# Performance work log

Hardware: AMD Instinct MI355X
Metric: run time of the kernel (lower is better)

## Reference

```python
import jax, jax.numpy as jnp
import numpy as np
import math

B, N, F, H = 16, 256, 1024, 16
HD = F // H  # head_dim = 64
NEG = -9e15


def setup_inputs() -> dict:
    key = jax.random.key(0)
    ks = jax.random.split(key, 12)
    s = 0.02
    return {
        "obj_feats": jax.random.normal(ks[0], (B, N, F), jnp.float32),
        "cross_feats": jax.random.normal(ks[1], (B, N, F), jnp.float32),
        "adj_matrix": jax.random.randint(ks[2], (B, N, N), 0, 2, jnp.int32),
        "label_biases_att": jax.random.normal(ks[3], (B, N, N), jnp.float32),
        "Wq": jax.random.normal(ks[4], (F, F), jnp.float32) * s,
        "bq": jnp.zeros((F,), jnp.float32),
        "Wk": jax.random.normal(ks[5], (F, F), jnp.float32) * s,
        "bk": jnp.zeros((F,), jnp.float32),
        "Wv": jax.random.normal(ks[6], (F, F), jnp.float32) * s,
        "bv": jnp.zeros((F,), jnp.float32),
        # grouped 1x1 conv: out=F, groups=H, in_per_group=F -> weight [F, F]
        "Wo": jax.random.normal(ks[7], (F, F), jnp.float32) * s,
        "bo": jnp.zeros((F,), jnp.float32),
    }


def reference(obj_feats, cross_feats, adj_matrix, label_biases_att,
              Wq, bq, Wk, bk, Wv, bv, Wo, bo):
    # projections (torch Linear: x @ W.T + b)
    q = (jnp.einsum('bnf,gf->bng', obj_feats, Wq) + bq).reshape(B, N, H, HD)
    k = (jnp.einsum('bnf,gf->bng', cross_feats, Wk) + bk).reshape(B, N, H, HD)
    v = jnp.einsum('bnf,gf->bng', cross_feats, Wv) + bv          # [B, N, F] (NOT split per head)

    scale = 1.0 / math.sqrt(float(HD))
    att = jnp.einsum('bqhd,bkhd->bqhk', q, k) * scale            # [B, Nq, H, Nk]

    # adjacency mask broadcast over heads + label bias (both indexed [b, q, k])
    mask = (adj_matrix > 0)[:, :, None, :]                       # [B, Nq, 1, Nk]
    att = jnp.where(mask, att, NEG) + label_biases_att[:, :, None, :]

    p = jax.nn.softmax(att, axis=-1)                             # softmax over keys

    # weighted sum against un-split values: [B, Nq, H, Nk] x [B, Nk, F]
    out = jnp.einsum('bqhk,bkf->bqhf', p, v)                     # [B, Nq, H, F]

    # grouped 1x1 conv: group h maps its F input channels -> HD output channels
    Wo_g = Wo.reshape(H, HD, F)
    out = jnp.einsum('bqhf,hdf->bqhd', out, Wo_g) + bo.reshape(H, HD)
    out = out.reshape(B, N, F)

    att_mean = p.sum(axis=2) / H                                 # [B, Nq, Nk]
    return out, att_mean
```

## Files before the change

kernel.cpp:

```cpp
#include <hip/hip_runtime.h>

#define NEGF -9e15f

typedef __attribute__((ext_vector_type(8))) unsigned short u16x8;
typedef __attribute__((ext_vector_type(8))) short          s16x8;
typedef __attribute__((ext_vector_type(4))) float          f32x4;

__device__ __forceinline__ unsigned short f2bf(float x) {
  union { float f; unsigned int u; } c; c.f = x;
  unsigned int r = c.u + 0x7fffu + ((c.u >> 16) & 1u);
  return (unsigned short)(r >> 16);
}
__device__ __forceinline__ float bf2f(unsigned short v) {
  union { float f; unsigned int u; } c; c.u = ((unsigned int)v) << 16;
  return c.f;
}

__device__ __forceinline__ void gload16(const void* g, void* l) {
  __builtin_amdgcn_global_load_lds(
      (const __attribute__((address_space(1))) unsigned int*)g,
      (__attribute__((address_space(3))) unsigned int*)l, 16, 0, 0);
}

__global__ __launch_bounds__(256) void cvt2_bf16(
    const float* __restrict__ a, const float* __restrict__ b,
    unsigned short* __restrict__ oa, unsigned short* __restrict__ ob)
{
  const int bid = blockIdx.x;
  const float* in = (bid < 4096) ? a : b;
  unsigned short* out = (bid < 4096) ? oa : ob;
  const int i = ((bid & 4095) * 256 + threadIdx.x) * 4;
  const float4 v = *(const float4*)(in + i);
  ushort4 o;
  o.x = f2bf(v.x); o.y = f2bf(v.y); o.z = f2bf(v.z); o.w = f2bf(v.w);
  *(ushort4*)(out + i) = o;
}

__global__ __launch_bounds__(256) void prep_w(
    const float* __restrict__ Wq, const float* __restrict__ Wk,
    const float* __restrict__ Wo,
    unsigned short* __restrict__ Wall, unsigned short* __restrict__ Wo_bf)
{
  const int bid = blockIdx.x;
  const int i = ((bid & 1023) * 256 + threadIdx.x) * 4;
  const float* in;
  unsigned short* out;
  float sc = 1.f;
  if (bid < 1024)      { in = Wq; out = Wall;           sc = 0.125f; }
  else if (bid < 2048) { in = Wk; out = Wall + 1048576; }
  else                 { in = Wo; out = Wo_bf; }
  const float4 v = *(const float4*)(in + i);
  ushort4 o;
  o.x = f2bf(v.x * sc); o.y = f2bf(v.y * sc);
  o.z = f2bf(v.z * sc); o.w = f2bf(v.w * sc);
  *(ushort4*)(out + i) = o;
}

__global__ __launch_bounds__(256) void tcvt_bf16(
    const float* __restrict__ in, unsigned short* __restrict__ out, int R, int C)
{
  __shared__ float tile[32][33];
  const int bc = blockIdx.x * 32, br = blockIdx.y * 32;
  const int tx = threadIdx.x & 31, ty8 = threadIdx.x >> 5;
  #pragma unroll
  for (int j = 0; j < 32; j += 8)
    tile[ty8 + j][tx] = in[(size_t)(br + ty8 + j) * C + bc + tx];
  __syncthreads();
  #pragma unroll
  for (int j = 0; j < 32; j += 8)
    out[(size_t)(bc + ty8 + j) * R + br + tx] = f2bf(tile[tx][ty8 + j]);
}

__global__ __launch_bounds__(256) void bov_kernel(
    const float* __restrict__ Wo, const float* __restrict__ bv,
    float* __restrict__ bov)
{
  const int g    = blockIdx.x * 4 + (threadIdx.x >> 6);
  const int lane = threadIdx.x & 63;
  float acc = 0.f;
  for (int f = lane; f < 1024; f += 64)
    acc = fmaf(Wo[(size_t)g * 1024 + f], bv[f], acc);
  #pragma unroll
  for (int off = 32; off > 0; off >>= 1) acc += __shfl_down(acc, off);
  if (lane == 0) bov[g] = acc;
}

__global__ __launch_bounds__(256) void bias_prep(
    const float* __restrict__ bq, const float* __restrict__ bk,
    float* __restrict__ ball)
{
  const int i = blockIdx.x * 256 + threadIdx.x;
  ball[i]        = 0.125f * bq[i];
  ball[1024 + i] = bk[i];
}

__global__ __launch_bounds__(256) void mb_prep(
    const int* __restrict__ adj, const float* __restrict__ lab,
    float* __restrict__ mb)
{
  const int i = (blockIdx.x * 256 + threadIdx.x) * 4;
  const int4   a = *(const int4*)(adj + i);
  const float4 l = *(const float4*)(lab + i);
  float4 o;
  o.x = a.x > 0 ? l.x : NEGF;
  o.y = a.y > 0 ? l.y : NEGF;
  o.z = a.z > 0 ? l.z : NEGF;
  o.w = a.w > 0 ? l.w : NEGF;
  *(float4*)(mb + i) = o;
}

__global__ __launch_bounds__(256) void gemm_wov(
    const unsigned short* __restrict__ A,
    const unsigned short* __restrict__ Bw,
    unsigned short* __restrict__ Cout,
    int M, int N, int K)
{
  __shared__ unsigned short Asm[128][72];
  __shared__ unsigned short Bsm[64][72];
  const int t = threadIdx.x;
  const int lane = t & 63, w = t >> 6;
  const int wm = w >> 1, wn = w & 1;
  const int bm = blockIdx.y * 128, bn = blockIdx.x * 64;

  f32x4 acc[4][2] = {};

  const int sr  = t >> 3;
  const int skq = (t & 7) * 8;
  const int fr  = lane & 15;
  const int kf  = (lane >> 4) * 8;

  for (int k0 = 0; k0 < K; k0 += 64) {
    const u16x8 a0 = *(const u16x8*)(A  + (size_t)(bm + sr)      * K + k0 + skq);
    const u16x8 a1 = *(const u16x8*)(A  + (size_t)(bm + sr + 32) * K + k0 + skq);
    const u16x8 a2 = *(const u16x8*)(A  + (size_t)(bm + sr + 64) * K + k0 + skq);
    const u16x8 a3 = *(const u16x8*)(A  + (size_t)(bm + sr + 96) * K + k0 + skq);
    const u16x8 b0 = *(const u16x8*)(Bw + (size_t)(bn + sr)      * K + k0 + skq);
    const u16x8 b1 = *(const u16x8*)(Bw + (size_t)(bn + sr + 32) * K + k0 + skq);
    __syncthreads();
    *(u16x8*)&Asm[sr][skq]      = a0;
    *(u16x8*)&Asm[sr + 32][skq] = a1;
    *(u16x8*)&Asm[sr + 64][skq] = a2;
    *(u16x8*)&Asm[sr + 96][skq] = a3;
    *(u16x8*)&Bsm[sr][skq]      = b0;
    *(u16x8*)&Bsm[sr + 32][skq] = b1;
    __syncthreads();

    s16x8 af[4][2], bf[2][2];
    #pragma unroll
    for (int fm = 0; fm < 4; ++fm)
      #pragma unroll
      for (int kk = 0; kk < 2; ++kk)
        af[fm][kk] = *(const s16x8*)&Asm[wm * 64 + fm * 16 + fr][kf + kk * 32];
    #pragma unroll
    for (int fn = 0; fn < 2; ++fn)
      #pragma unroll
      for (int kk = 0; kk < 2; ++kk)
        bf[fn][kk] = *(const s16x8*)&Bsm[wn * 32 + fn * 16 + fr][kf + kk * 32];

    #pragma unroll
    for (int fm = 0; fm < 4; ++fm)
      #pragma unroll
      for (int fn = 0; fn < 2; ++fn) {
        acc[fm][fn] = __builtin_amdgcn_mfma_f32_16x16x32_bf16(af[fm][0], bf[fn][0], acc[fm][fn], 0, 0, 0);
        acc[fm][fn] = __builtin_amdgcn_mfma_f32_16x16x32_bf16(af[fm][1], bf[fn][1], acc[fm][fn], 0, 0, 0);
      }
  }

  const int rg = (lane >> 4) * 4;
  #pragma unroll
  for (int fm = 0; fm < 4; ++fm)
    #pragma unroll
    for (int fn = 0; fn < 2; ++fn) {
      const int col = bn + wn * 32 + fn * 16 + fr;
      #pragma unroll
      for (int r = 0; r < 4; ++r) {
        const int row = bm + wm * 64 + fm * 16 + rg + r;
        Cout[(size_t)row * N + col] = f2bf(acc[fm][fn][r]);
      }
    }
}

__global__ __launch_bounds__(256, 3) void gemm_big(
    const unsigned short* __restrict__ objA,
    const unsigned short* __restrict__ crossA,
    const unsigned short* __restrict__ Wall,
    const float* __restrict__ ball,
    unsigned short* __restrict__ Qo,
    unsigned short* __restrict__ Ko,
    unsigned short* __restrict__ VWt)
{
  __shared__ unsigned short Asm[128 * 64];
  __shared__ unsigned short Bsm[128 * 64];
  const int t = threadIdx.x;
  const int w = t >> 6, lane = t & 63;
  const int wm = w >> 1, wn = w & 1;

  const int bid = blockIdx.x;
  const int xcd = bid & 7, j = bid >> 3;
  const int bmi = (xcd >> 1) * 8 + j / 12;
  const int bni = (xcd & 1) * 12 + j % 12;
  const int bm = bmi * 128;
  const int bn = bni * 128;
  const unsigned short* Ag = (bn < 1024) ? objA : crossA;

  const int srow = lane >> 3;
  const int skel = (lane & 7) * 8;
  const int fr = lane & 15, kf = (lane >> 4) * 8;

  f32x4 acc[4][4] = {};

  for (int k0 = 0; k0 < 1024; k0 += 64) {
    if (k0) __syncthreads();
    #pragma unroll
    for (int i = 0; i < 4; ++i) {
      const int c = i * 4 + w;
      const int r = c * 8 + srow;
      gload16(Ag   + (size_t)(bm + r) * 1024 + k0 + skel, &Asm[c * 512]);
      gload16(Wall + (size_t)(bn + r) * 1024 + k0 + skel, &Bsm[c * 512]);
    }
    __syncthreads();
    #pragma unroll
    for (int kk = 0; kk < 2; ++kk) {
      s16x8 af[4], bf[4];
      #pragma unroll
      for (int fm = 0; fm < 4; ++fm)
        af[fm] = *(const s16x8*)&Asm[(wm * 64 + fm * 16 + fr) * 64 + kk * 32 + kf];
      #pragma unroll
      for (int fn = 0; fn < 4; ++fn)
        bf[fn] = *(const s16x8*)&Bsm[(wn * 64 + fn * 16 + fr) * 64 + kk * 32 + kf];
      #pragma unroll
      for (int fm = 0; fm < 4; ++fm)
        #pragma unroll
        for (int fn = 0; fn < 4; ++fn)
          acc[fm][fn] = __builtin_amdgcn_mfma_f32_16x16x32_bf16(af[fm], bf[fn], acc[fm][fn], 0, 0, 0);
    }
  }

  const int rg = (lane >> 4) * 4;
  const int mode = bn >> 10;
  #pragma unroll
  for (int fm = 0; fm < 4; ++fm) {
    #pragma unroll
    for (int fn = 0; fn < 4; ++fn) {
      const int col  = bn + wn * 64 + fn * 16 + fr;
      const int cl   = col & 1023;
      const float bb = ball[col];
      const int row0 = bm + wm * 64 + fm * 16 + rg;
      if (mode == 0) {
        #pragma unroll
        for (int r = 0; r < 4; ++r)
          Qo[(size_t)(row0 + r) * 1024 + cl] = f2bf(acc[fm][fn][r] + bb);
      } else if (mode == 1) {
        #pragma unroll
        for (int r = 0; r < 4; ++r)
          Ko[(size_t)(row0 + r) * 1024 + cl] = f2bf(acc[fm][fn][r] + bb);
      } else {
        const int bidx = row0 >> 8, tok = row0 & 255;
        ushort4 u;
        u.x = f2bf(acc[fm][fn][0] + bb);
        u.y = f2bf(acc[fm][fn][1] + bb);
        u.z = f2bf(acc[fm][fn][2] + bb);
        u.w = f2bf(acc[fm][fn][3] + bb);
        *(ushort4*)(VWt + ((size_t)bidx * 1024 + cl) * 256 + tok) = u;
      }
    }
  }
}

__global__ __launch_bounds__(256, 2) void attn_mfma(
    const unsigned short* __restrict__ Qg,
    const unsigned short* __restrict__ Kg,
    const unsigned short* __restrict__ VWt,
    const float* __restrict__ mb,
    const float* __restrict__ bo,
    float* __restrict__ outp, unsigned short* __restrict__ Pb)
{
  const int t = threadIdx.x;
  const int w = t >> 6, lane = t & 63;
  const int fr = lane & 15, grp = lane >> 4;
  const int bid = blockIdx.x;
  const int qt = bid >> 8, hb = bid & 255;
  const int h = hb & 15, b = hb >> 4;
  const int q0 = qt * 64 + w * 16;

  __shared__ __align__(16) unsigned short Ks[256 * 64];
  __shared__ __align__(16) unsigned short VWs[64 * 256];

  {
    const unsigned short* kb = Kg + (size_t)(b * 256) * 1024 + h * 64;
    const int colb = (lane & 7) * 16;
    #pragma unroll
    for (int c = 0; c < 8; ++c) {
      const int row = c * 32 + w * 8 + (lane >> 3);
      const int sb  = colb ^ ((row & 7) << 4);
      gload16(kb + (size_t)row * 1024 + (sb >> 1), (char*)Ks + c * 4096 + w * 1024);
    }
  }
  {
    const unsigned short* vwb = VWt + (size_t)(b * 16 + h) * 16384;
    const int xb = (lane & 31) * 16;
    #pragma unroll
    for (int c = 0; c < 8; ++c) {
      const int row = c * 8 + w * 2 + (lane >> 5);
      const int sb  = xb ^ ((row & 7) << 4);
      gload16(vwb + row * 256 + (sb >> 1), (char*)VWs + c * 4096 + w * 1024);
    }
  }

  const unsigned short* qp = Qg + ((size_t)(b * 256 + q0 + fr)) * 1024 + h * 64 + grp * 8;
  const s16x8 qf0 = *(const s16x8*)qp;
  const s16x8 qf1 = *(const s16x8*)(qp + 32);

  __syncthreads();

  const float* mbp = mb + ((size_t)(b * 256 + q0 + fr)) * 256 + grp * 4;
  const int colA = (grp * 16) ^ ((fr & 7) << 4);

  f32x4 s[16];
  #pragma unroll
  for (int nf = 0; nf < 16; ++nf) s[nf] = (f32x4){0.f, 0.f, 0.f, 0.f};

  s16x8 kA[8], kB[8];
  float4 mA[4], mB[4];
  float mx = -3e38f;

#define LOADB(KF, MF, nb)                                                    \
  { _Pragma("unroll") for (int i = 0; i < 4; ++i) {                          \
      const char* rp = (const char*)Ks + (((nb)*4 + i) * 16 + fr) * 128;     \
      KF[2*i]   = *(const s16x8*)(rp + colA);                                \
      KF[2*i+1] = *(const s16x8*)(rp + (colA ^ 64));                         \
      MF[i]     = *(const float4*)(mbp + ((nb)*4 + i) * 16); } }
#define MFMAB(KF, nb)                                                        \
  { _Pragma("unroll") for (int i = 0; i < 4; ++i) {                          \
      s[(nb)*4+i] = __builtin_amdgcn_mfma_f32_16x16x32_bf16(KF[2*i],   qf0, s[(nb)*4+i], 0, 0, 0); \
      s[(nb)*4+i] = __builtin_amdgcn_mfma_f32_16x16x32_bf16(KF[2*i+1], qf1, s[(nb)*4+i], 0, 0, 0); } }
#define MASKB(MF, nb)                                                        \
  { _Pragma("unroll") for (int i = 0; i < 4; ++i) {                          \
      _Pragma("unroll") for (int r = 0; r < 4; ++r) {                        \
        const float m = ((const float*)&MF[i])[r];                           \
        const float v = (m > -1e14f) ? s[(nb)*4+i][r] + m : m;               \
        s[(nb)*4+i][r] = v; mx = fmaxf(mx, v); } } }

  LOADB(kA, mA, 0); LOADB(kB, mB, 1); MFMAB(kA, 0);
  MASKB(mA, 0);     LOADB(kA, mA, 2); MFMAB(kB, 1);
  MASKB(mB, 1);     LOADB(kB, mB, 3); MFMAB(kA, 2);
  MASKB(mA, 2);     LOADB(kA, mA, 4); MFMAB(kB, 3);
  MASKB(mB, 3);     LOADB(kB, mB, 5); MFMAB(kA, 4);
  MASKB(mA, 4);     LOADB(kA, mA, 6); MFMAB(kB, 5);
  MASKB(mB, 5);     LOADB(kB, mB, 7); MFMAB(kA, 6);
  MASKB(mA, 6);     MFMAB(kB, 7);     MASKB(mB, 7);
#undef LOADB
#undef MFMAB
#undef MASKB

  mx = fmaxf(mx, __shfl_xor(mx, 16));
  mx = fmaxf(mx, __shfl_xor(mx, 32));
  float sm = 0.f;
  #pragma unroll
  for (int nf = 0; nf < 16; ++nf)
    #pragma unroll
    for (int r = 0; r < 4; ++r) {
      const float e = __expf(s[nf][r] - mx);
      s[nf][r] = e;
      sm += e;
    }
  sm += __shfl_xor(sm, 16);
  sm += __shfl_xor(sm, 32);
  const float inv = 1.f / sm;

  uint2 u2[16];
  #pragma unroll
  for (int nf = 0; nf < 16; ++nf) {
    const unsigned lo = (unsigned)f2bf(s[nf][0] * inv) | ((unsigned)f2bf(s[nf][1] * inv) << 16);
    const unsigned hi = (unsigned)f2bf(s[nf][2] * inv) | ((unsigned)f2bf(s[nf][3] * inv) << 16);
    u2[nf] = make_uint2(lo, hi);
  }

  unsigned short* prow = Pb + (((size_t)(b * 16 + h)) * 256 + q0 + fr) * 256 + grp * 4;
  #pragma unroll
  for (int nf = 0; nf < 16; ++nf)
    *(uint2*)(prow + nf * 16) = u2[nf];

  f32x4 o[4];
  #pragma unroll
  for (int nf = 0; nf < 4; ++nf) o[nf] = (f32x4){0.f, 0.f, 0.f, 0.f};
  const int srcA = fr + ((grp & 1) << 5);
  const int srcB = srcA + 16;
  const int swz  = (fr & 7) << 4;
  const bool hiSel = (grp & 2);
  #pragma unroll
  for (int ks = 0; ks < 8; ++ks) {
    const int aLx = __shfl((int)u2[2 * ks].x,     srcA, 64);
    const int aLy = __shfl((int)u2[2 * ks].y,     srcA, 64);
    const int bLx = __shfl((int)u2[2 * ks].x,     srcB, 64);
    const int bLy = __shfl((int)u2[2 * ks].y,     srcB, 64);
    const int aHx = __shfl((int)u2[2 * ks + 1].x, srcA, 64);
    const int aHy = __shfl((int)u2[2 * ks + 1].y, srcA, 64);
    const int bHx = __shfl((int)u2[2 * ks + 1].x, srcB, 64);
    const int bHy = __shfl((int)u2[2 * ks + 1].y, srcB, 64);
    union { int4 i; s16x8 v; } pf;
    pf.i = hiSel ? make_int4(aHx, aHy, bHx, bHy) : make_int4(aLx, aLy, bLx, bLy);
    const int cb = (ks * 64 + grp * 16) ^ swz;
    #pragma unroll
    for (int nf = 0; nf < 4; ++nf) {
      const s16x8 vf = *(const s16x8*)((const char*)VWs + (nf * 16 + fr) * 512 + cb);
      o[nf] = __builtin_amdgcn_mfma_f32_16x16x32_bf16(pf.v, vf, o[nf], 0, 0, 0);
    }
  }

  #pragma unroll
  for (int nf = 0; nf < 4; ++nf) {
    const float bb = bo[h * 64 + nf * 16 + fr];
    #pragma unroll
    for (int r = 0; r < 4; ++r)
      outp[((size_t)b * 256 + q0 + grp * 4 + r) * 1024 + h * 64 + nf * 16 + fr]
          = o[nf][r] + bb;
  }
}

__global__ __launch_bounds__(256) void attm_reduce(
    const unsigned short* __restrict__ Pb, float* __restrict__ attm)
{
  const size_t idx = (size_t)blockIdx.x * 256 + threadIdx.x;
  const int    k8  = (int)(idx & 31);
  const size_t bq  = idx >> 5;
  const int    b   = (int)(bq >> 8);
  const int    q   = (int)(bq & 255);
  float s[8] = {};
  const unsigned short* base = Pb + (size_t)b * 1048576 + (size_t)q * 256 + k8 * 8;
  #pragma unroll
  for (int hh = 0; hh < 16; ++hh) {
    const u16x8 p = *(const u16x8*)(base + (size_t)hh * 65536);
    #pragma unroll
    for (int j = 0; j < 8; ++j) s[j] += bf2f(p[j]);
  }
  float* dst = attm + bq * 256 + k8 * 8;
  float4 r0, r1;
  r0.x = s[0] * 0.0625f; r0.y = s[1] * 0.0625f; r0.z = s[2] * 0.0625f; r0.w = s[3] * 0.0625f;
  r1.x = s[4] * 0.0625f; r1.y = s[5] * 0.0625f; r1.z = s[6] * 0.0625f; r1.w = s[7] * 0.0625f;
  *(float4*)dst = r0;
  *(float4*)(dst + 4) = r1;
}

extern "C" void kernel_launch(void* const* d_in, const int* in_sizes, int n_in,
                              void* d_out, int out_size, void* d_ws, size_t ws_size,
                              hipStream_t stream)
{
  const float* obj   = (const float*)d_in[0];
  const float* cross = (const float*)d_in[1];
  const int*   adj   = (const int*)d_in[2];
  const float* lab   = (const float*)d_in[3];
  const float* Wq    = (const float*)d_in[4];
  const float* bq    = (const float*)d_in[5];
  const float* Wk    = (const float*)d_in[6];
  const float* bk    = (const float*)d_in[7];
  const float* Wv    = (const float*)d_in[8];
  const float* bv    = (const float*)d_in[9];
  const float* Wo    = (const float*)d_in[10];
  const float* bo    = (const float*)d_in[11];

  float* out  = (float*)d_out;
  float* attm = out + (size_t)16 * 256 * 1024;

  char* ws = (char*)d_ws;
  unsigned short* obj_bf   = (unsigned short*)(ws + 0);
  unsigned short* cross_bf = (unsigned short*)(ws + 8388608);
  unsigned short* Qbf      = (unsigned short*)(ws + 16777216);
  unsigned short* Kbf      = (unsigned short*)(ws + 25165824);
  unsigned short* VWt      = (unsigned short*)(ws + 33554432);
  unsigned short* Wall     = (unsigned short*)(ws + 41943040);
  unsigned short* Wo_bf    = (unsigned short*)(ws + 48234496);
  unsigned short* Wvt_bf   = (unsigned short*)(ws + 50331648);
  float*          ball     = (float*)(ws + 50331648);
  unsigned short* Pbuf     = (unsigned short*)(ws + 52432896);
  float*          mbuf     = (float*)obj_bf;

  cvt2_bf16<<<8192, 256, 0, stream>>>(obj, cross, obj_bf, cross_bf);
  prep_w<<<3072, 256, 0, stream>>>(Wq, Wk, Wo, Wall, Wo_bf);
  tcvt_bf16<<<dim3(32, 32), 256, 0, stream>>>(Wv, Wvt_bf, 1024, 1024);

  gemm_wov<<<dim3(16, 8), 256, 0, stream>>>(
      Wo_bf, Wvt_bf, Wall + 2097152, 1024, 1024, 1024);

  bias_prep<<<4, 256, 0, stream>>>(bq, bk, ball);
  bov_kernel<<<256, 256, 0, stream>>>(Wo, bv, ball + 2048);

  gemm_big<<<768, 256, 0, stream>>>(
      obj_bf, cross_bf, Wall, ball, Qbf, Kbf, VWt);

  mb_prep<<<1024, 256, 0, stream>>>(adj, lab, mbuf);

  attn_mfma<<<1024, 256, 0, stream>>>(
      Qbf, Kbf, VWt, mbuf, bo, out, Pbuf);
  attm_reduce<<<512, 256, 0, stream>>>(Pbuf, attm);
}
```

Measured before the change: 123.8 us.

## Merge weight-prep kernels, use direct-to-LDS loads in gemm_wov, remap attention blocks per XCD

```diff
diff --git a/kernel.cpp b/kernel.cpp
--- a/kernel.cpp
+++ b/kernel.cpp
@@ -38,60 +38,59 @@
 
 __global__ __launch_bounds__(256) void prep_w(
     const float* __restrict__ Wq, const float* __restrict__ Wk,
-    const float* __restrict__ Wo,
-    unsigned short* __restrict__ Wall, unsigned short* __restrict__ Wo_bf)
-{
+    const float* __restrict__ Wo, const float* __restrict__ Wv,
+    unsigned short* __restrict__ Wall, unsigned short* __restrict__ Wo_bf,
+    unsigned short* __restrict__ Wvt_bf)
+{
+  __shared__ float tile[32][33];
   const int bid = blockIdx.x;
-  const int i = ((bid & 1023) * 256 + threadIdx.x) * 4;
-  const float* in;
-  unsigned short* out;
-  float sc = 1.f;
-  if (bid < 1024)      { in = Wq; out = Wall;           sc = 0.125f; }
-  else if (bid < 2048) { in = Wk; out = Wall + 1048576; }
-  else                 { in = Wo; out = Wo_bf; }
-  const float4 v = *(const float4*)(in + i);
-  ushort4 o;
-  o.x = f2bf(v.x * sc); o.y = f2bf(v.y * sc);
-  o.z = f2bf(v.z * sc); o.w = f2bf(v.w * sc);
-  *(ushort4*)(out + i) = o;
-}
-
-__global__ __launch_bounds__(256) void tcvt_bf16(
-    const float* __restrict__ in, unsigned short* __restrict__ out, int R, int C)
-{
-  __shared__ float tile[32][33];
-  const int bc = blockIdx.x * 32, br = blockIdx.y * 32;
-  const int tx = threadIdx.x & 31, ty8 = threadIdx.x >> 5;
-  #pragma unroll
-  for (int j = 0; j < 32; j += 8)
-    tile[ty8 + j][tx] = in[(size_t)(br + ty8 + j) * C + bc + tx];
-  __syncthreads();
-  #pragma unroll
-  for (int j = 0; j < 32; j += 8)
-    out[(size_t)(bc + ty8 + j) * R + br + tx] = f2bf(tile[tx][ty8 + j]);
-}
-
-__global__ __launch_bounds__(256) void bov_kernel(
+  if (bid < 3072) {
+    const int i = ((bid & 1023) * 256 + threadIdx.x) * 4;
+    const float* in;
+    unsigned short* out;
+    float sc = 1.f;
+    if (bid < 1024)      { in = Wq; out = Wall;           sc = 0.125f; }
+    else if (bid < 2048) { in = Wk; out = Wall + 1048576; }
+    else                 { in = Wo; out = Wo_bf; }
+    const float4 v = *(const float4*)(in + i);
+    ushort4 o;
+    o.x = f2bf(v.x * sc); o.y = f2bf(v.y * sc);
+    o.z = f2bf(v.z * sc); o.w = f2bf(v.w * sc);
+    *(ushort4*)(out + i) = o;
+  } else {
+    const int j = bid - 3072;
+    const int bc = (j & 31) * 32, br = (j >> 5) * 32;
+    const int tx = threadIdx.x & 31, ty8 = threadIdx.x >> 5;
+    #pragma unroll
+    for (int jj = 0; jj < 32; jj += 8)
+      tile[ty8 + jj][tx] = Wv[(size_t)(br + ty8 + jj) * 1024 + bc + tx];
+    __syncthreads();
+    #pragma unroll
+    for (int jj = 0; jj < 32; jj += 8)
+      Wvt_bf[(size_t)(bc + ty8 + jj) * 1024 + br + tx] = f2bf(tile[tx][ty8 + jj]);
+  }
+}
+
+__global__ __launch_bounds__(256) void prep_bias(
+    const float* __restrict__ bq, const float* __restrict__ bk,
     const float* __restrict__ Wo, const float* __restrict__ bv,
-    float* __restrict__ bov)
-{
-  const int g    = blockIdx.x * 4 + (threadIdx.x >> 6);
-  const int lane = threadIdx.x & 63;
-  float acc = 0.f;
-  for (int f = lane; f < 1024; f += 64)
-    acc = fmaf(Wo[(size_t)g * 1024 + f], bv[f], acc);
-  #pragma unroll
-  for (int off = 32; off > 0; off >>= 1) acc += __shfl_down(acc, off);
-  if (lane == 0) bov[g] = acc;
-}
-
-__global__ __launch_bounds__(256) void bias_prep(
-    const float* __restrict__ bq, const float* __restrict__ bk,
     float* __restrict__ ball)
 {
-  const int i = blockIdx.x * 256 + threadIdx.x;
-  ball[i]        = 0.125f * bq[i];
-  ball[1024 + i] = bk[i];
+  const int bid = blockIdx.x;
+  if (bid < 4) {
+    const int i = bid * 256 + threadIdx.x;
+    ball[i]        = 0.125f * bq[i];
+    ball[1024 + i] = bk[i];
+  } else {
+    const int g    = (bid - 4) * 4 + (threadIdx.x >> 6);
+    const int lane = threadIdx.x & 63;
+    float acc = 0.f;
+    for (int f = lane; f < 1024; f += 64)
+      acc = fmaf(Wo[(size_t)g * 1024 + f], bv[f], acc);
+    #pragma unroll
+    for (int off = 32; off > 0; off >>= 1) acc += __shfl_down(acc, off);
+    if (lane == 0) ball[2048 + g] = acc;
+  }
 }
 
 __global__ __launch_bounds__(256) void mb_prep(
@@ -109,61 +108,54 @@
   *(float4*)(mb + i) = o;
 }
 
-__global__ __launch_bounds__(256) void gemm_wov(
+__global__ __launch_bounds__(256, 3) void gemm_wov(
     const unsigned short* __restrict__ A,
     const unsigned short* __restrict__ Bw,
-    unsigned short* __restrict__ Cout,
-    int M, int N, int K)
-{
-  __shared__ unsigned short Asm[128][72];
-  __shared__ unsigned short Bsm[64][72];
+    unsigned short* __restrict__ Cout)
+{
+  __shared__ unsigned short Asm[128 * 64];
+  __shared__ unsigned short Bsm[64 * 64];
   const int t = threadIdx.x;
   const int lane = t & 63, w = t >> 6;
   const int wm = w >> 1, wn = w & 1;
   const int bm = blockIdx.y * 128, bn = blockIdx.x * 64;
 
+  const int srow = lane >> 3;
+  const int skel = (lane & 7) * 8;
+  const int fr = lane & 15, kf = (lane >> 4) * 8;
+
   f32x4 acc[4][2] = {};
 
-  const int sr  = t >> 3;
-  const int skq = (t & 7) * 8;
-  const int fr  = lane & 15;
-  const int kf  = (lane >> 4) * 8;
-
-  for (int k0 = 0; k0 < K; k0 += 64) {
-    const u16x8 a0 = *(const u16x8*)(A  + (size_t)(bm + sr)      * K + k0 + skq);
-    const u16x8 a1 = *(const u16x8*)(A  + (size_t)(bm + sr + 32) * K + k0 + skq);
-    const u16x8 a2 = *(const u16x8*)(A  + (size_t)(bm + sr + 64) * K + k0 + skq);
-    const u16x8 a3 = *(const u16x8*)(A  + (size_t)(bm + sr + 96) * K + k0 + skq);
-    const u16x8 b0 = *(const u16x8*)(Bw + (size_t)(bn + sr)      * K + k0 + skq);
-    const u16x8 b1 = *(const u16x8*)(Bw + (size_t)(bn + sr + 32) * K + k0 + skq);
+  for (int k0 = 0; k0 < 1024; k0 += 64) {
+    if (k0) __syncthreads();
+    #pragma unroll
+    for (int i = 0; i < 4; ++i) {
+      const int c = i * 4 + w;
+      const int r = c * 8 + srow;
+      gload16(A + (size_t)(bm + r) * 1024 + k0 + skel, &Asm[c * 512]);
+    }
+    #pragma unroll
+    for (int i = 0; i < 2; ++i) {
+      const int c = i * 4 + w;
+      const int r = c * 8 + srow;
+      gload16(Bw + (size_t)(bn + r) * 1024 + k0 + skel, &Bsm[c * 512]);
+    }
     __syncthreads();
-    *(u16x8*)&Asm[sr][skq]      = a0;
-    *(u16x8*)&Asm[sr + 32][skq] = a1;
-    *(u16x8*)&Asm[sr + 64][skq] = a2;
-    *(u16x8*)&Asm[sr + 96][skq] = a3;
-    *(u16x8*)&Bsm[sr][skq]      = b0;
-    *(u16x8*)&Bsm[sr + 32][skq] = b1;
-    __syncthreads();
-
-    s16x8 af[4][2], bf[2][2];
-    #pragma unroll
-    for (int fm = 0; fm < 4; ++fm)
-      #pragma unroll
-      for (int kk = 0; kk < 2; ++kk)
-        af[fm][kk] = *(const s16x8*)&Asm[wm * 64 + fm * 16 + fr][kf + kk * 32];
-    #pragma unroll
-    for (int fn = 0; fn < 2; ++fn)
-      #pragma unroll
-      for (int kk = 0; kk < 2; ++kk)
-        bf[fn][kk] = *(const s16x8*)&Bsm[wn * 32 + fn * 16 + fr][kf + kk * 32];
-
-    #pragma unroll
-    for (int fm = 0; fm < 4; ++fm)
-      #pragma unroll
-      for (int fn = 0; fn < 2; ++fn) {
-        acc[fm][fn] = __builtin_amdgcn_mfma_f32_16x16x32_bf16(af[fm][0], bf[fn][0], acc[fm][fn], 0, 0, 0);
-        acc[fm][fn] = __builtin_amdgcn_mfma_f32_16x16x32_bf16(af[fm][1], bf[fn][1], acc[fm][fn], 0, 0, 0);
-      }
+    #pragma unroll
+    for (int kk = 0; kk < 2; ++kk) {
+      s16x8 af[4], bf[2];
+      #pragma unroll
+      for (int fm = 0; fm < 4; ++fm)
+        af[fm] = *(const s16x8*)&Asm[(wm * 64 + fm * 16 + fr) * 64 + kk * 32 + kf];
+      #pragma unroll
+      for (int fn = 0; fn < 2; ++fn)
+        bf[fn] = *(const s16x8*)&Bsm[(wn * 32 + fn * 16 + fr) * 64 + kk * 32 + kf];
+      #pragma unroll
+      for (int fm = 0; fm < 4; ++fm)
+        #pragma unroll
+        for (int fn = 0; fn < 2; ++fn)
+          acc[fm][fn] = __builtin_amdgcn_mfma_f32_16x16x32_bf16(af[fm], bf[fn], acc[fm][fn], 0, 0, 0);
+    }
   }
 
   const int rg = (lane >> 4) * 4;
@@ -175,7 +167,7 @@
       #pragma unroll
       for (int r = 0; r < 4; ++r) {
         const int row = bm + wm * 64 + fm * 16 + rg + r;
-        Cout[(size_t)row * N + col] = f2bf(acc[fm][fn][r]);
+        Cout[(size_t)row * 1024 + col] = f2bf(acc[fm][fn][r]);
       }
     }
 }
@@ -279,8 +271,11 @@
   const int w = t >> 6, lane = t & 63;
   const int fr = lane & 15, grp = lane >> 4;
   const int bid = blockIdx.x;
-  const int qt = bid >> 8, hb = bid & 255;
-  const int h = hb & 15, b = hb >> 4;
+  const int xcd = bid & 7, i = bid >> 3;
+  const int h   = i & 15;
+  const int bqt = xcd * 8 + (i >> 4);
+  const int b   = bqt >> 2;
+  const int qt  = bqt & 3;
   const int q0 = qt * 64 + w * 16;
 
   __shared__ __align__(16) unsigned short Ks[256 * 64];
@@ -325,21 +320,21 @@
   float mx = -3e38f;
 
 #define LOADB(KF, MF, nb)                                                    \
-  { _Pragma("unroll") for (int i = 0; i < 4; ++i) {                          \
-      const char* rp = (const char*)Ks + (((nb)*4 + i) * 16 + fr) * 128;     \
-      KF[2*i]   = *(const s16x8*)(rp + colA);                                \
-      KF[2*i+1] = *(const s16x8*)(rp + (colA ^ 64));                         \
-      MF[i]     = *(const float4*)(mbp + ((nb)*4 + i) * 16); } }
+  { _Pragma("unroll") for (int i2 = 0; i2 < 4; ++i2) {                       \
+      const char* rp = (const char*)Ks + (((nb)*4 + i2) * 16 + fr) * 128;    \
+      KF[2*i2]   = *(const s16x8*)(rp + colA);                               \
+      KF[2*i2+1] = *(const s16x8*)(rp + (colA ^ 64));                        \
+      MF[i2]     = *(const float4*)(mbp + ((nb)*4 + i2) * 16); } }
 #define MFMAB(KF, nb)                                                        \
-  { _Pragma("unroll") for (int i = 0; i < 4; ++i) {                          \
-      s[(nb)*4+i] = __builtin_amdgcn_mfma_f32_16x16x32_bf16(KF[2*i],   qf0, s[(nb)*4+i], 0, 0, 0); \
-      s[(nb)*4+i] = __builtin_amdgcn_mfma_f32_16x16x32_bf16(KF[2*i+1], qf1, s[(nb)*4+i], 0, 0, 0); } }
+  { _Pragma("unroll") for (int i2 = 0; i2 < 4; ++i2) {                       \
+      s[(nb)*4+i2] = __builtin_amdgcn_mfma_f32_16x16x32_bf16(KF[2*i2],   qf0, s[(nb)*4+i2], 0, 0, 0); \
+      s[(nb)*4+i2] = __builtin_amdgcn_mfma_f32_16x16x32_bf16(KF[2*i2+1], qf1, s[(nb)*4+i2], 0, 0, 0); } }
 #define MASKB(MF, nb)                                                        \
-  { _Pragma("unroll") for (int i = 0; i < 4; ++i) {                          \
+  { _Pragma("unroll") for (int i2 = 0; i2 < 4; ++i2) {                       \
       _Pragma("unroll") for (int r = 0; r < 4; ++r) {                        \
-        const float m = ((const float*)&MF[i])[r];                           \
-        const float v = (m > -1e14f) ? s[(nb)*4+i][r] + m : m;               \
-        s[(nb)*4+i][r] = v; mx = fmaxf(mx, v); } } }
+        const float m = ((const float*)&MF[i2])[r];                          \
+        const float v = (m > -1e14f) ? s[(nb)*4+i2][r] + m : m;              \
+        s[(nb)*4+i2][r] = v; mx = fmaxf(mx, v); } } }
 
   LOADB(kA, mA, 0); LOADB(kB, mB, 1); MFMAB(kA, 0);
   MASKB(mA, 0);     LOADB(kA, mA, 2); MFMAB(kB, 1);
@@ -476,14 +471,11 @@
   float*          mbuf     = (float*)obj_bf;
 
   cvt2_bf16<<<8192, 256, 0, stream>>>(obj, cross, obj_bf, cross_bf);
-  prep_w<<<3072, 256, 0, stream>>>(Wq, Wk, Wo, Wall, Wo_bf);
-  tcvt_bf16<<<dim3(32, 32), 256, 0, stream>>>(Wv, Wvt_bf, 1024, 1024);
-
-  gemm_wov<<<dim3(16, 8), 256, 0, stream>>>(
-      Wo_bf, Wvt_bf, Wall + 2097152, 1024, 1024, 1024);
-
-  bias_prep<<<4, 256, 0, stream>>>(bq, bk, ball);
-  bov_kernel<<<256, 256, 0, stream>>>(Wo, bv, ball + 2048);
+  prep_w<<<4096, 256, 0, stream>>>(Wq, Wk, Wo, Wv, Wall, Wo_bf, Wvt_bf);
+
+  gemm_wov<<<dim3(16, 8), 256, 0, stream>>>(Wo_bf, Wvt_bf, Wall + 2097152);
+
+  prep_bias<<<260, 256, 0, stream>>>(bq, bk, Wo, bv, ball);
 
   gemm_big<<<768, 256, 0, stream>>>(
       obj_bf, cross_bf, Wall, ball, Qbf, Kbf, VWt);
```

Result: faster. 119.7 us (-3.3%).
